# Optimization experiments

Hardware: AMD Instinct MI355X
Metric: run time of the kernel (lower is better)

Reference implementation:

```python
import jax, jax.numpy as jnp
import numpy as np

B, LR_DIM, G_DIM, K, D, T = 256, 1024, 512, 64, 256, 8
GRID = jnp.linspace(-4.0, 4.0, 41)  # registered buffer in torch module


def _mu_bell(x, c, a_bell, b_bell):
    # generalized bell membership, clamp(a,b) >= 1e-3 as in torch
    a = jnp.maximum(a_bell, 1e-3)
    b = jnp.maximum(b_bell, 1e-3)
    return 1.0 / (1.0 + jnp.abs((x - c) / a) ** (2.0 * b))


def _mu_s(x, a, b):
    eps = 1e-12
    a2 = jnp.minimum(a, b)
    b2 = jnp.maximum(a, b)
    mid = (a2 + b2) * 0.5
    up = 2.0 * ((x - a2) / (b2 - a2 + eps)) ** 2
    dn = 1.0 - 2.0 * ((b2 - x) / (b2 - a2 + eps)) ** 2
    y = jnp.where((x > a2) & (x <= mid), up, jnp.zeros_like(x))
    y = jnp.where((x > mid) & (x <= b2), dn, y)
    return jnp.where(x > b2, jnp.ones_like(x), y)


def _fuzzify(x, a_bell, b_bell):
    # x: (B,d) -> (B,2d)
    xs = 4.0 * jnp.tanh(x / 4.0)
    xb = _mu_bell(xs, 0.0, a_bell, b_bell)
    xS = _mu_s(xs, -1.0, 1.0)
    return jnp.concatenate([xb, xS], axis=-1)


def _defuzzify(rt, a_bell, b_bell):
    # rt: (B,2d) -> centroid (B,d)
    d = rt.shape[1] // 2
    rb, rs = rt[:, :d], rt[:, d:]
    g = GRID[None, None, :]                      # (1,1,G)
    c_b = 4.0 * jnp.tanh(rb)[..., None]          # (B,d,1)
    c_s = 4.0 * jnp.tanh(rs)[..., None]
    mu_b = _mu_bell(g, c_b, a_bell, b_bell)      # (B,d,G)
    a_s = jnp.clip(c_s - 1.0, -4.0, 4.0)
    b_s = jnp.clip(c_s + 1.0, -4.0, 4.0)
    mu_s = _mu_s(g, a_s, b_s)
    cen_b = (g * mu_b).sum(-1) / (mu_b.sum(-1) + 1e-12)
    cen_s = (g * mu_s).sum(-1) / (mu_s.sum(-1) + 1e-12)
    return 0.5 * cen_b + 0.5 * cen_s


def _forward(wsi_lr, genomics, FT, W_lr, b_lr, W_g, b_g, WqI, WqG, WkI, WkG,
             WvI, WvG, mlp_W1, mlp_b1, mlp_W2, mlp_b2, Wf, bf, Wi, bi, Vf, Vi,
             a_bell, b_bell):
    scale = jnp.float32(D) ** 0.5
    lr = wsi_lr @ W_lr + b_lr                    # (B,d)
    g = genomics @ W_g + b_g
    lr_f = _fuzzify(lr, a_bell, b_bell)          # (B,2d)
    g_f = _fuzzify(g, a_bell, b_bell)
    QI = lr_f @ WqI                              # (B,d), loop-invariant
    QG = g_f @ WqG
    Ft0 = jnp.broadcast_to(FT[None], (wsi_lr.shape[0],) + FT.shape)  # (B,K,d)

    def step(Ft, _):
        sI = jnp.einsum('bd,bkd->bk', QI, Ft @ WkI) / scale
        sG = jnp.einsum('bd,bkd->bk', QG, Ft @ WkG) / scale
        rtI = jnp.einsum('bk,bke->be', jax.nn.softmax(sI, axis=-1), Ft @ WvI)  # (B,2d)
        rtG = jnp.einsum('bk,bke->be', jax.nn.softmax(sG, axis=-1), Ft @ WvG)
        r = 0.5 * _defuzzify(rtI, a_bell, b_bell) + 0.5 * _defuzzify(rtG, a_bell, b_bell)
        rb = jnp.broadcast_to(r[:, None, :], Ft.shape)              # (B,K,d)
        x = Ft + rb
        F_tilde = jax.nn.gelu(x @ mlp_W1 + mlp_b1, approximate=False) @ mlp_W2 + mlp_b2 + x
        f_gate = jax.nn.sigmoid(rb @ Wf + bf + jnp.tanh(Ft @ Vf))
        i_gate = jax.nn.sigmoid(rb @ Wi + bi + jnp.tanh(Ft @ Vi))
        Ft_new = f_gate * Ft + i_gate * jnp.tanh(F_tilde)
        return Ft_new, Ft_new

    _, steps = jax.lax.scan(step, Ft0, None, length=T)
    # torch stores step `T-s` result at index s-1: list index 0 holds the LAST
    # computed state, index T-1 the first -> reverse chronological order
    return steps[::-1]  # (T,B,K,d)


def setup_inputs() -> dict:
    key = jax.random.key(0)
    ks = jax.random.split(key, 20)

    def rn(k, shape, scale):
        return jax.random.normal(k, shape, dtype=jnp.float32) * scale

    z = lambda *s: jnp.zeros(s, jnp.float32)
    return dict(
        wsi_lr=rn(ks[0], (B, LR_DIM), 1.0),
        genomics=rn(ks[1], (B, G_DIM), 1.0),
        FT=rn(ks[2], (K, D), 0.02),
        W_lr=rn(ks[3], (LR_DIM, D), LR_DIM ** -0.5), b_lr=z(D),
        W_g=rn(ks[4], (G_DIM, D), G_DIM ** -0.5), b_g=z(D),
        WqI=rn(ks[5], (2 * D, D), (2 * D) ** -0.5),
        WqG=rn(ks[6], (2 * D, D), (2 * D) ** -0.5),
        WkI=rn(ks[7], (D, D), D ** -0.5),
        WkG=rn(ks[8], (D, D), D ** -0.5),
        WvI=rn(ks[9], (D, 2 * D), D ** -0.5),
        WvG=rn(ks[10], (D, 2 * D), D ** -0.5),
        mlp_W1=rn(ks[11], (D, 2 * D), D ** -0.5), mlp_b1=z(2 * D),
        mlp_W2=rn(ks[12], (2 * D, D), (2 * D) ** -0.5), mlp_b2=z(D),
        Wf=rn(ks[13], (D, D), D ** -0.5), bf=z(D),
        Wi=rn(ks[14], (D, D), D ** -0.5), bi=z(D),
        Vf=rn(ks[15], (D, D), D ** -0.5),
        Vi=rn(ks[16], (D, D), D ** -0.5),
        a_bell=jnp.float32(1.0),
        b_bell=jnp.float32(2.0),
    )


def reference(wsi_lr, genomics, FT, W_lr, b_lr, W_g, b_g, WqI, WqG, WkI, WkG,
              WvI, WvG, mlp_W1, mlp_b1, mlp_W2, mlp_b2, Wf, bf, Wi, bi, Vf, Vi,
              a_bell, b_bell):
    return _forward(wsi_lr, genomics, FT, W_lr, b_lr, W_g, b_g, WqI, WqG, WkI,
                    WkG, WvI, WvG, mlp_W1, mlp_b1, mlp_W2, mlp_b2, Wf, bf, Wi,
                    bi, Vf, Vi, a_bell, b_bell)
```

## Files before the change

kernel.cpp:

```cpp
#include <hip/hip_runtime.h>
#include <hip/hip_bf16.h>

#define B_    256
#define K_    64
#define D_    256
#define T_    8
#define NROW  (B_*K_)

typedef short short8v __attribute__((ext_vector_type(8)));
typedef float f32x4  __attribute__((ext_vector_type(4)));

__device__ __forceinline__ float fexp2(float x) { return __builtin_amdgcn_exp2f(x); }
__device__ __forceinline__ float flog2(float x) { return __builtin_amdgcn_logf(x); }

__device__ __forceinline__ float sigmoid_f(float x) {
  return 1.f / (1.f + fexp2(x * -1.4426950408889634f));
}
__device__ __forceinline__ float tanh_fast(float x) {
  float xc = fminf(fmaxf(x, -30.f), 30.f);
  float t = fexp2(xc * 2.8853900817779268f);
  return (t - 1.f) / (t + 1.f);
}
__device__ __forceinline__ float gelu_f(float x) {
  return 0.5f * x * (1.f + erff(x * 0.70710678118654752440f));
}
__device__ __forceinline__ unsigned short f2bf(float x) {
  __hip_bfloat16 h = __float2bfloat16(x);
  return *reinterpret_cast<unsigned short*>(&h);
}
__device__ __forceinline__ float bfss(unsigned short s) {
  return __uint_as_float(((unsigned int)s) << 16);
}
__device__ __forceinline__ float muS_f(float x, float a2, float b2) {
  float mid = 0.5f * (a2 + b2);
  float inv = 1.f / (b2 - a2 + 1e-12f);
  if (x > b2)  return 1.f;
  if (x > mid) { float u = (b2 - x) * inv; return 1.f - 2.f * u * u; }
  if (x > a2)  { float u = (x - a2) * inv; return 2.f * u * u; }
  return 0.f;
}
__device__ __forceinline__ float pow_abs(float z, float e2b) {
  return fexp2(e2b * flog2(fabsf(z)));
}
__device__ __forceinline__ float defuzz_one(float rb_, float rs_, float ab, float bb) {
  float e2b = 2.f * bb;
  float inv_ab = 1.f / ab;
  float cb = 4.f * tanh_fast(rb_);
  float num = 0.f, den = 0.f;
  #pragma unroll
  for (int j = 0; j < 41; ++j) {
    float gj = -4.f + 0.2f * (float)j;
    float mu = 1.f / (1.f + pow_abs((gj - cb) * inv_ab, e2b));
    num += gj * mu; den += mu;
  }
  float cenb = num / (den + 1e-12f);
  float cs = 4.f * tanh_fast(rs_);
  float as_ = fminf(fmaxf(cs - 1.f, -4.f), 4.f);
  float bs_ = fminf(fmaxf(cs + 1.f, -4.f), 4.f);
  num = 0.f; den = 0.f;
  {
    float mid = 0.5f * (as_ + bs_);
    float inv = 1.f / (bs_ - as_ + 1e-12f);
    #pragma unroll
    for (int j = 0; j < 41; ++j) {
      float gj = -4.f + 0.2f * (float)j;
      float mu;
      if (gj > bs_)      mu = 1.f;
      else if (gj > mid) { float u = (bs_ - gj) * inv; mu = 1.f - 2.f * u * u; }
      else if (gj > as_) { float u = (gj - as_) * inv; mu = 2.f * u * u; }
      else               mu = 0.f;
      num += gj * mu; den += mu;
    }
  }
  float cens = num / (den + 1e-12f);
  return 0.5f * cenb + 0.5f * cens;
}

__global__ __launch_bounds__(256) void k_convert(
    const float* __restrict__ W1, const float* __restrict__ Vf, const float* __restrict__ Vi,
    const float* __restrict__ W2, const float* __restrict__ FT,
    const float* __restrict__ WkI, const float* __restrict__ WkG,
    const float* __restrict__ WvI, const float* __restrict__ WvG,
    const float* __restrict__ Wf,  const float* __restrict__ Wi,
    unsigned short* __restrict__ B1t, unsigned short* __restrict__ W2t,
    unsigned short* __restrict__ FTbf,
    float* __restrict__ WkIt, float* __restrict__ WkGt,
    unsigned short* __restrict__ Wv2, unsigned short* __restrict__ WB)
{
  int idx = blockIdx.x * 256 + threadIdx.x;
  if (idx < 262144) {
    int n = idx >> 8, k = idx & 255;
    float v = (n < 512) ? W1[(size_t)k*512 + n]
            : (n < 768) ? Vf[(size_t)k*256 + (n-512)]
                        : Vi[(size_t)k*256 + (n-768)];
    B1t[idx] = f2bf(v);
  } else if (idx < 393216) {
    int j = idx - 262144;
    int n = j >> 9, k = j & 511;
    W2t[j] = f2bf(W2[(size_t)k*256 + n]);
  } else if (idx < 409600) {
    int j = idx - 393216;
    FTbf[j] = f2bf(FT[j]);
  } else if (idx < 475136) {
    int j = idx - 409600;
    int k = j >> 8, n = j & 255;
    WkIt[j] = WkI[(size_t)n*256 + k];
  } else if (idx < 540672) {
    int j = idx - 475136;
    int k = j >> 8, n = j & 255;
    WkGt[j] = WkG[(size_t)n*256 + k];
  } else if (idx < 802816) {
    int j = idx - 540672;
    int d = j >> 10, c = j & 1023;
    float v = (c < 512) ? WvI[(size_t)d*512 + c] : WvG[(size_t)d*512 + (c-512)];
    Wv2[j] = f2bf(v);
  } else if (idx < 1064960) {
    int j = idx - 802816;
    int d = j >> 10, c = j & 1023;
    float v = (c < 512) ? W1[(size_t)d*512 + c]
            : (c < 768) ? Wf[(size_t)d*256 + (c-512)]
                        : Wi[(size_t)d*256 + (c-768)];
    WB[j] = f2bf(v);
  }
}

__global__ __launch_bounds__(256) void k_pre_lin(
    const float* __restrict__ wsi, const float* __restrict__ gen,
    const float* __restrict__ W_lr, const float* __restrict__ b_lr,
    const float* __restrict__ W_g,  const float* __restrict__ b_g,
    const float* __restrict__ a_p,  const float* __restrict__ b_p,
    float* __restrict__ lrf, float* __restrict__ gf)
{
  int g_ix = blockIdx.x;
  int half = g_ix >> 4, tile = g_ix & 15;
  int bx = tile & 3, by = tile >> 2;
  int n0 = bx * 64, m0 = by * 64;
  const float* A    = half ? gen  : wsi;
  const float* Bm   = half ? W_g  : W_lr;
  const float* bias = half ? b_g  : b_lr;
  float* outp       = half ? gf   : lrf;
  int KK            = half ? 512  : 1024;
  float ab = fmaxf(a_p[0], 0.001f), bb = fmaxf(b_p[0], 0.001f);
  float e2b = 2.f * bb, inv_ab = 1.f / ab;

  __shared__ float As[16][64];
  __shared__ float Bs[16][64];
  int tid = threadIdx.x, tx = tid & 15, ty = tid >> 4;
  float acc[4][4] = {};
  int am = tid >> 2, ak = (tid & 3) * 4;
  int bk = tid >> 4, bn = (tid & 15) * 4;
  const float* arow = A + (size_t)(m0 + am) * KK;
  for (int k0 = 0; k0 < KK; k0 += 16) {
    float4 av = *(const float4*)(arow + k0 + ak);
    As[ak+0][am] = av.x; As[ak+1][am] = av.y; As[ak+2][am] = av.z; As[ak+3][am] = av.w;
    *(float4*)&Bs[bk][bn] = *(const float4*)(Bm + (size_t)(k0 + bk) * 256 + n0 + bn);
    __syncthreads();
    #pragma unroll
    for (int kk = 0; kk < 16; ++kk) {
      float a0 = As[kk][ty*4+0], a1 = As[kk][ty*4+1], a2 = As[kk][ty*4+2], a3 = As[kk][ty*4+3];
      float b0 = Bs[kk][tx*4+0], b1 = Bs[kk][tx*4+1], b2 = Bs[kk][tx*4+2], b3 = Bs[kk][tx*4+3];
      acc[0][0]=fmaf(a0,b0,acc[0][0]); acc[0][1]=fmaf(a0,b1,acc[0][1]); acc[0][2]=fmaf(a0,b2,acc[0][2]); acc[0][3]=fmaf(a0,b3,acc[0][3]);
      acc[1][0]=fmaf(a1,b0,acc[1][0]); acc[1][1]=fmaf(a1,b1,acc[1][1]); acc[1][2]=fmaf(a1,b2,acc[1][2]); acc[1][3]=fmaf(a1,b3,acc[1][3]);
      acc[2][0]=fmaf(a2,b0,acc[2][0]); acc[2][1]=fmaf(a2,b1,acc[2][1]); acc[2][2]=fmaf(a2,b2,acc[2][2]); acc[2][3]=fmaf(a2,b3,acc[2][3]);
      acc[3][0]=fmaf(a3,b0,acc[3][0]); acc[3][1]=fmaf(a3,b1,acc[3][1]); acc[3][2]=fmaf(a3,b2,acc[3][2]); acc[3][3]=fmaf(a3,b3,acc[3][3]);
    }
    __syncthreads();
  }
  #pragma unroll
  for (int i = 0; i < 4; ++i) {
    int row = m0 + ty*4 + i;
    #pragma unroll
    for (int j = 0; j < 4; ++j) {
      int col = n0 + tx*4 + j;
      float v = acc[i][j] + bias[col];
      float xs = 4.f * tanh_fast(v * 0.25f);
      outp[(size_t)row*512 + col]       = 1.f / (1.f + pow_abs(xs * inv_ab, e2b));
      outp[(size_t)row*512 + col + 256] = muS_f(xs, -1.f, 1.f);
    }
  }
}

__global__ __launch_bounds__(256) void k_pre_q(
    const float* __restrict__ lrf, const float* __restrict__ gf,
    const float* __restrict__ WqI, const float* __restrict__ WqG,
    float* __restrict__ QI, float* __restrict__ QG)
{
  int g_ix = blockIdx.x;
  int half = g_ix >> 4, tile = g_ix & 15;
  int bx = tile & 3, by = tile >> 2;
  int n0 = bx * 64, m0 = by * 64;
  const float* A  = half ? gf  : lrf;
  const float* Bm = half ? WqG : WqI;
  float* outp     = half ? QG  : QI;

  __shared__ float As[16][64];
  __shared__ float Bs[16][64];
  int tid = threadIdx.x, tx = tid & 15, ty = tid >> 4;
  float acc[4][4] = {};
  int am = tid >> 2, ak = (tid & 3) * 4;
  int bk = tid >> 4, bn = (tid & 15) * 4;
  const float* arow = A + (size_t)(m0 + am) * 512;
  for (int k0 = 0; k0 < 512; k0 += 16) {
    float4 av = *(const float4*)(arow + k0 + ak);
    As[ak+0][am] = av.x; As[ak+1][am] = av.y; As[ak+2][am] = av.z; As[ak+3][am] = av.w;
    *(float4*)&Bs[bk][bn] = *(const float4*)(Bm + (size_t)(k0 + bk) * 256 + n0 + bn);
    __syncthreads();
    #pragma unroll
    for (int kk = 0; kk < 16; ++kk) {
      float a0 = As[kk][ty*4+0], a1 = As[kk][ty*4+1], a2 = As[kk][ty*4+2], a3 = As[kk][ty*4+3];
      float b0 = Bs[kk][tx*4+0], b1 = Bs[kk][tx*4+1], b2 = Bs[kk][tx*4+2], b3 = Bs[kk][tx*4+3];
      acc[0][0]=fmaf(a0,b0,acc[0][0]); acc[0][1]=fmaf(a0,b1,acc[0][1]); acc[0][2]=fmaf(a0,b2,acc[0][2]); acc[0][3]=fmaf(a0,b3,acc[0][3]);
      acc[1][0]=fmaf(a1,b0,acc[1][0]); acc[1][1]=fmaf(a1,b1,acc[1][1]); acc[1][2]=fmaf(a1,b2,acc[1][2]); acc[1][3]=fmaf(a1,b3,acc[1][3]);
      acc[2][0]=fmaf(a2,b0,acc[2][0]); acc[2][1]=fmaf(a2,b1,acc[2][1]); acc[2][2]=fmaf(a2,b2,acc[2][2]); acc[2][3]=fmaf(a2,b3,acc[2][3]);
      acc[3][0]=fmaf(a3,b0,acc[3][0]); acc[3][1]=fmaf(a3,b1,acc[3][1]); acc[3][2]=fmaf(a3,b2,acc[3][2]); acc[3][3]=fmaf(a3,b3,acc[3][3]);
    }
    __syncthreads();
  }
  #pragma unroll
  for (int i = 0; i < 4; ++i) {
    float4 v = make_float4(acc[i][0], acc[i][1], acc[i][2], acc[i][3]);
    *(float4*)(outp + (size_t)(m0 + ty*4 + i) * 256 + n0 + tx*4) = v;
  }
}

__global__ __launch_bounds__(256) void k_pre_qp(
    const float* __restrict__ QI, const float* __restrict__ QG,
    const float* __restrict__ WkIt, const float* __restrict__ WkGt,
    float* __restrict__ qIp, float* __restrict__ qGp)
{
  int g_ix = blockIdx.x;
  int half = g_ix >> 4, tile = g_ix & 15;
  int bx = tile & 3, by = tile >> 2;
  int n0 = bx * 64, m0 = by * 64;
  const float* A  = half ? QG   : QI;
  const float* Bm = half ? WkGt : WkIt;
  float* outp     = half ? qGp  : qIp;

  __shared__ float As[16][64];
  __shared__ float Bs[16][64];
  int tid = threadIdx.x, tx = tid & 15, ty = tid >> 4;
  float acc[4][4] = {};
  int am = tid >> 2, ak = (tid & 3) * 4;
  int bk = tid >> 4, bn = (tid & 15) * 4;
  const float* arow = A + (size_t)(m0 + am) * 256;
  for (int k0 = 0; k0 < 256; k0 += 16) {
    float4 av = *(const float4*)(arow + k0 + ak);
    As[ak+0][am] = av.x; As[ak+1][am] = av.y; As[ak+2][am] = av.z; As[ak+3][am] = av.w;
    *(float4*)&Bs[bk][bn] = *(const float4*)(Bm + (size_t)(k0 + bk) * 256 + n0 + bn);
    __syncthreads();
    #pragma unroll
    for (int kk = 0; kk < 16; ++kk) {
      float a0 = As[kk][ty*4+0], a1 = As[kk][ty*4+1], a2 = As[kk][ty*4+2], a3 = As[kk][ty*4+3];
      float b0 = Bs[kk][tx*4+0], b1 = Bs[kk][tx*4+1], b2 = Bs[kk][tx*4+2], b3 = Bs[kk][tx*4+3];
      acc[0][0]=fmaf(a0,b0,acc[0][0]); acc[0][1]=fmaf(a0,b1,acc[0][1]); acc[0][2]=fmaf(a0,b2,acc[0][2]); acc[0][3]=fmaf(a0,b3,acc[0][3]);
      acc[1][0]=fmaf(a1,b0,acc[1][0]); acc[1][1]=fmaf(a1,b1,acc[1][1]); acc[1][2]=fmaf(a1,b2,acc[1][2]); acc[1][3]=fmaf(a1,b3,acc[1][3]);
      acc[2][0]=fmaf(a2,b0,acc[2][0]); acc[2][1]=fmaf(a2,b1,acc[2][1]); acc[2][2]=fmaf(a2,b2,acc[2][2]); acc[2][3]=fmaf(a2,b3,acc[2][3]);
      acc[3][0]=fmaf(a3,b0,acc[3][0]); acc[3][1]=fmaf(a3,b1,acc[3][1]); acc[3][2]=fmaf(a3,b2,acc[3][2]); acc[3][3]=fmaf(a3,b3,acc[3][3]);
    }
    __syncthreads();
  }
  #pragma unroll
  for (int i = 0; i < 4; ++i) {
    float4 v = make_float4(acc[i][0], acc[i][1], acc[i][2], acc[i][3]);
    *(float4*)(outp + (size_t)(m0 + ty*4 + i) * 256 + n0 + tx*4) = v;
  }
}

__global__ __launch_bounds__(512) void k_scan(
    const unsigned short* __restrict__ FTbf, const float* __restrict__ FTf,
    const float* __restrict__ qIp, const float* __restrict__ qGp,
    const unsigned short* __restrict__ Wv2, const unsigned short* __restrict__ WB,
    const float* __restrict__ b1, const float* __restrict__ bfv,
    const float* __restrict__ biv, const float* __restrict__ b2,
    const unsigned short* __restrict__ B1t, const unsigned short* __restrict__ W2t,
    const float* __restrict__ a_p, const float* __restrict__ b_p,
    unsigned short* __restrict__ Gf, unsigned short* __restrict__ Gi,
    float* __restrict__ out)
{
  __shared__ __align__(16) short Fs[64*264];
  __shared__ __align__(16) short Bstage[64*264];
  __shared__ __align__(16) short Wstage[256*72];
  __shared__ __align__(16) short A2ch[64*72];
  __shared__ float qv[512];
  __shared__ float red[512];
  __shared__ float prl[128];
  __shared__ float ftb[512];
  __shared__ float rL[256];
  __shared__ float rWall[1024];

  int b = blockIdx.x, tid = threadIdx.x;
  int w = tid >> 6, lane = tid & 63, lr = lane & 15, lh = lane >> 4;
  int rg = w & 3, cg = w >> 2;
  float ab = fmaxf(a_p[0], 0.001f), bb = fmaxf(b_p[0], 0.001f);

  #pragma unroll
  for (int p = 0; p < 4; ++p) {
    int idx = (p*512 + tid) * 8;
    int row = idx >> 8, col = idx & 255;
    *(float4*)&Fs[row*264 + col] = *(const float4*)&FTbf[idx];
  }
  qv[tid] = (tid < 256) ? qIp[(size_t)b*256 + tid] : qGp[(size_t)b*256 + tid - 256];
  __syncthreads();

  const float* Fprev = nullptr;
  for (int st = 0; st < T_; ++st) {
    float* Fout = out + (size_t)(7 - st) * NROW * 256;

    {
      int which = tid >> 8, tt = tid & 255, k = tt & 63, part = tt >> 6;
      const unsigned int* frow = (const unsigned int*)&Fs[k*264 + part*64];
      const float* q0 = qv + which*256 + part*64;
      float s0 = 0.f;
      #pragma unroll
      for (int d2 = 0; d2 < 32; ++d2) {
        unsigned int pr = frow[d2];
        float f0 = __uint_as_float(pr << 16);
        float f1 = __uint_as_float(pr & 0xffff0000u);
        s0 = fmaf(f1, q0[2*d2+1], fmaf(f0, q0[2*d2], s0));
      }
      red[which*256 + tt] = s0;
    }
    __syncthreads();
    if (tid < 128) {
      int which = tid >> 6, kk = tid & 63;
      const float* rp = red + which*256;
      float s = (rp[kk] + rp[64+kk] + rp[128+kk] + rp[192+kk]) * (1.f/16.f);
      float m = s;
      for (int off = 32; off; off >>= 1) m = fmaxf(m, __shfl_xor(m, off, 64));
      float e = fexp2((s - m) * 1.4426950408889634f);
      float sum = e;
      for (int off = 32; off; off >>= 1) sum += __shfl_xor(sum, off, 64);
      prl[which*64 + kk] = e / sum;
    }
    __syncthreads();
    {
      int which = tid >> 8, tt = tid & 255;
      const float* pp = prl + which*64;
      float f0 = 0.f;
      #pragma unroll 8
      for (int kk = 0; kk < 64; ++kk)
        f0 = fmaf(pp[kk], bfss((unsigned short)Fs[kk*264 + tt]), f0);
      ftb[which*256 + tt] = f0;
    }
    __syncthreads();
    {
      int half = tid >> 8, tt = tid & 255;
      const float* fb = ftb + half*256;
      const unsigned short* wv = Wv2 + half*512 + tt;
      float a0 = 0.f, a1 = 0.f;
      #pragma unroll 4
      for (int d = 0; d < 256; ++d) {
        float fv = fb[d];
        a0 = fmaf(fv, bfss(wv[(size_t)d*1024]),       a0);
        a1 = fmaf(fv, bfss(wv[(size_t)d*1024 + 256]), a1);
      }
      red[half*256 + tt] = defuzz_one(a0, a1, ab, bb);
    }
    __syncthreads();
    if (tid < 256) rL[tid] = 0.5f * (red[tid] + red[256 + tid]);
    __syncthreads();
    {
      float w0 = 0.f, w1 = 0.f;
      const unsigned short* wb0 = WB + tid;
      #pragma unroll 4
      for (int d = 0; d < 256; ++d) {
        float rv = rL[d];
        w0 = fmaf(rv, bfss(wb0[(size_t)d*1024]),       w0);
        w1 = fmaf(rv, bfss(wb0[(size_t)d*1024 + 512]), w1);
      }
      rWall[tid]       = w0 + b1[tid];
      rWall[512 + tid] = w1 + ((tid < 256) ? bfv[tid] : biv[tid - 256]);
    }
    __syncthreads();

    for (int c = 8; c < 16; ++c) {
      #pragma unroll
      for (int p = 0; p < 4; ++p) {
        int idx = (p*512 + tid) * 8;
        int row = idx >> 8, col = idx & 255;
        *(float4*)&Bstage[row*264 + col] = *(const float4*)&B1t[(size_t)c*16384 + idx];
      }
      __syncthreads();
      #pragma unroll
      for (int f = 0; f < 2; ++f) {
        f32x4 acc = {0.f,0.f,0.f,0.f};
        int nb = cg*32 + f*16;
        #pragma unroll
        for (int ks = 0; ks < 8; ++ks) {
          short8v av = *(const short8v*)&Fs[(rg*16 + lr)*264 + ks*32 + lh*8];
          short8v bv = *(const short8v*)&Bstage[(nb + lr)*264 + ks*32 + lh*8];
          acc = __builtin_amdgcn_mfma_f32_16x16x32_bf16(av, bv, acc, 0, 0, 0);
        }
        int gc = c*64 + nb + lr;
        float add = rWall[gc];
        int cc = gc - 512;
        #pragma unroll
        for (int r = 0; r < 4; ++r) {
          int row = b*64 + rg*16 + lh*4 + r;
          unsigned short val = f2bf(sigmoid_f(add + tanh_fast(acc[r])));
          if (cc < 256) Gf[(size_t)row*256 + cc]       = val;
          else          Gi[(size_t)row*256 + cc - 256] = val;
        }
      }
      __syncthreads();
    }

    f32x4 O[8];
    #pragma unroll
    for (int nn = 0; nn < 8; ++nn) { O[nn][0]=0.f; O[nn][1]=0.f; O[nn][2]=0.f; O[nn][3]=0.f; }
    for (int c = 0; c < 8; ++c) {
      #pragma unroll
      for (int p = 0; p < 4; ++p) {
        int idx = (p*512 + tid) * 8;
        int row = idx >> 8, col = idx & 255;
        *(float4*)&Bstage[row*264 + col] = *(const float4*)&B1t[(size_t)c*16384 + idx];
      }
      #pragma unroll
      for (int p = 0; p < 4; ++p) {
        int idx = (p*512 + tid) * 8;
        int n = idx >> 6, kk = idx & 63;
        *(float4*)&Wstage[n*72 + kk] = *(const float4*)&W2t[(size_t)n*512 + c*64 + kk];
      }
      __syncthreads();
      #pragma unroll
      for (int f = 0; f < 2; ++f) {
        f32x4 acc = {0.f,0.f,0.f,0.f};
        int nb = cg*32 + f*16;
        #pragma unroll
        for (int ks = 0; ks < 8; ++ks) {
          short8v av = *(const short8v*)&Fs[(rg*16 + lr)*264 + ks*32 + lh*8];
          short8v bv = *(const short8v*)&Bstage[(nb + lr)*264 + ks*32 + lh*8];
          acc = __builtin_amdgcn_mfma_f32_16x16x32_bf16(av, bv, acc, 0, 0, 0);
        }
        int gc = c*64 + nb + lr;
        float add = rWall[gc];
        #pragma unroll
        for (int r = 0; r < 4; ++r)
          A2ch[(rg*16 + lh*4 + r)*72 + nb + lr] = f2bf(gelu_f(acc[r] + add));
      }
      __syncthreads();
      #pragma unroll
      for (int ks2 = 0; ks2 < 2; ++ks2) {
        short8v av = *(const short8v*)&A2ch[(rg*16 + lr)*72 + ks2*32 + lh*8];
        #pragma unroll
        for (int nn = 0; nn < 8; ++nn) {
          short8v bv = *(const short8v*)&Wstage[(cg*128 + nn*16 + lr)*72 + ks2*32 + lh*8];
          O[nn] = __builtin_amdgcn_mfma_f32_16x16x32_bf16(av, bv, O[nn], 0, 0, 0);
        }
      }
      __syncthreads();
    }

    #pragma unroll
    for (int nn = 0; nn < 8; ++nn) {
      int col = cg*128 + nn*16 + lr;
      float b2c = b2[col], rv = rL[col];
      #pragma unroll
      for (int r = 0; r < 4; ++r) {
        int rowl = rg*16 + lh*4 + r;
        int row = b*64 + rowl;
        float Ftv = (st == 0) ? FTf[rowl*256 + col] : Fprev[(size_t)row*256 + col];
        float ftld = O[nn][r] + b2c + Ftv + rv;
        float fg = bfss(Gf[(size_t)row*256 + col]);
        float ig = bfss(Gi[(size_t)row*256 + col]);
        float ov = fg * Ftv + ig * tanh_fast(ftld);
        Fout[(size_t)row*256 + col] = ov;
        Fs[rowl*264 + col] = f2bf(ov);
      }
    }
    Fprev = Fout;
    __syncthreads();
  }
}

extern "C" void kernel_launch(void* const* d_in, const int* in_sizes, int n_in,
                              void* d_out, int out_size, void* d_ws, size_t ws_size,
                              hipStream_t stream)
{
  (void)in_sizes; (void)n_in; (void)out_size; (void)ws_size;
  const float* wsi  = (const float*)d_in[0];
  const float* gen  = (const float*)d_in[1];
  const float* FT   = (const float*)d_in[2];
  const float* W_lr = (const float*)d_in[3];
  const float* b_lr = (const float*)d_in[4];
  const float* W_g  = (const float*)d_in[5];
  const float* b_g  = (const float*)d_in[6];
  const float* WqI  = (const float*)d_in[7];
  const float* WqG  = (const float*)d_in[8];
  const float* WkI  = (const float*)d_in[9];
  const float* WkG  = (const float*)d_in[10];
  const float* WvI  = (const float*)d_in[11];
  const float* WvG  = (const float*)d_in[12];
  const float* W1   = (const float*)d_in[13];
  const float* b1   = (const float*)d_in[14];
  const float* W2   = (const float*)d_in[15];
  const float* b2   = (const float*)d_in[16];
  const float* Wf   = (const float*)d_in[17];
  const float* bf   = (const float*)d_in[18];
  const float* Wi   = (const float*)d_in[19];
  const float* bi   = (const float*)d_in[20];
  const float* Vf   = (const float*)d_in[21];
  const float* Vi   = (const float*)d_in[22];
  const float* a_p  = (const float*)d_in[23];
  const float* b_p  = (const float*)d_in[24];

  float* out = (float*)d_out;
  float* ws  = (float*)d_ws;
  float* qIp   = ws;
  float* qGp   = qIp   + 65536;
  float* lrf   = qGp   + 65536;
  float* gf    = lrf   + 131072;
  float* QI    = gf    + 131072;
  float* QG    = QI    + 65536;
  float* WkIt  = QG    + 65536;
  float* WkGt  = WkIt  + 65536;
  unsigned short* Gfb  = (unsigned short*)(WkGt + 65536);
  unsigned short* Gib  = Gfb  + 4194304;
  unsigned short* FTbf = Gib  + 4194304;
  unsigned short* B1t  = FTbf + 16384;
  unsigned short* W2t  = B1t  + 262144;
  unsigned short* Wv2  = W2t  + 131072;
  unsigned short* WB   = Wv2  + 262144;

  k_convert<<<4160, 256, 0, stream>>>(W1, Vf, Vi, W2, FT, WkI, WkG, WvI, WvG, Wf, Wi,
                                      B1t, W2t, FTbf, WkIt, WkGt, Wv2, WB);
  k_pre_lin<<<32, 256, 0, stream>>>(wsi, gen, W_lr, b_lr, W_g, b_g, a_p, b_p, lrf, gf);
  k_pre_q<<<32, 256, 0, stream>>>(lrf, gf, WqI, WqG, QI, QG);
  k_pre_qp<<<32, 256, 0, stream>>>(QI, QG, WkIt, WkGt, qIp, qGp);

  k_scan<<<256, 512, 0, stream>>>(FTbf, FT, qIp, qGp, Wv2, WB,
                                  b1, bf, bi, b2, B1t, W2t, a_p, b_p,
                                  Gfb, Gib, out);
}
```

Measured before the change: 870.3 us.

## Prefetch next weight chunk into registers during MFMA loops; stagger score reads

The gate and MLP chunk loops now load the next chunk of B1t (and W2t) from global memory into registers right after the barrier, so the global loads overlap with the current chunk's MFMA work instead of stalling before each LDS store. The attention score loop also rotates its start index by k to spread LDS bank accesses. The change adds register pressure (8 extra float4 per thread in the MLP loop), which could lower occupancy or cause spills.

```diff
diff --git a/kernel.cpp b/kernel.cpp
--- a/kernel.cpp
+++ b/kernel.cpp
@@ -312,7 +312,8 @@
       const float* q0 = qv + which*256 + part*64;
       float s0 = 0.f;
       #pragma unroll
-      for (int d2 = 0; d2 < 32; ++d2) {
+      for (int d2i = 0; d2i < 32; ++d2i) {
+        int d2 = (d2i + k) & 31;
         unsigned int pr = frow[d2];
         float f0 = __uint_as_float(pr << 16);
         float f1 = __uint_as_float(pr & 0xffff0000u);
@@ -369,86 +370,113 @@
         w1 = fmaf(rv, bfss(wb0[(size_t)d*1024 + 512]), w1);
       }
       rWall[tid]       = w0 + b1[tid];
-      rWall[512 + tid] = w1 + ((tid < 256) ? bfv[tid] : biv[tid - 256]);
-    }
-    __syncthreads();
-
-    for (int c = 8; c < 16; ++c) {
+      int tt = tid & 255;
+      rWall[512 + tid] = w1 + ((tid < 256) ? bfv[tt] : biv[tt]);
+    }
+    __syncthreads();
+
+    {
+      float4 pfB[4];
+      #pragma unroll
+      for (int p = 0; p < 4; ++p)
+        pfB[p] = *(const float4*)&B1t[(size_t)8*16384 + (p*512 + tid)*8];
+      for (int c = 8; c < 16; ++c) {
+        #pragma unroll
+        for (int p = 0; p < 4; ++p) {
+          int idx = (p*512 + tid) * 8;
+          int row = idx >> 8, col = idx & 255;
+          *(float4*)&Bstage[row*264 + col] = pfB[p];
+        }
+        __syncthreads();
+        if (c < 15) {
+          #pragma unroll
+          for (int p = 0; p < 4; ++p)
+            pfB[p] = *(const float4*)&B1t[(size_t)(c+1)*16384 + (p*512 + tid)*8];
+        }
+        #pragma unroll
+        for (int f = 0; f < 2; ++f) {
+          f32x4 acc = {0.f,0.f,0.f,0.f};
+          int nb = cg*32 + f*16;
+          #pragma unroll
+          for (int ks = 0; ks < 8; ++ks) {
+            short8v av = *(const short8v*)&Fs[(rg*16 + lr)*264 + ks*32 + lh*8];
+            short8v bv = *(const short8v*)&Bstage[(nb + lr)*264 + ks*32 + lh*8];
+            acc = __builtin_amdgcn_mfma_f32_16x16x32_bf16(av, bv, acc, 0, 0, 0);
+          }
+          int gc = c*64 + nb + lr;
+          float add = rWall[gc];
+          int cc = gc - 512;
+          #pragma unroll
+          for (int r = 0; r < 4; ++r) {
+            int row = b*64 + rg*16 + lh*4 + r;
+            unsigned short val = f2bf(sigmoid_f(add + tanh_fast(acc[r])));
+            if (cc < 256) Gf[(size_t)row*256 + cc]       = val;
+            else          Gi[(size_t)row*256 + cc - 256] = val;
+          }
+        }
+        __syncthreads();
+      }
+    }
+
+    f32x4 O[8];
+    #pragma unroll
+    for (int nn = 0; nn < 8; ++nn) { O[nn][0]=0.f; O[nn][1]=0.f; O[nn][2]=0.f; O[nn][3]=0.f; }
+    {
+      float4 pfB[4], pfW[4];
       #pragma unroll
       for (int p = 0; p < 4; ++p) {
         int idx = (p*512 + tid) * 8;
-        int row = idx >> 8, col = idx & 255;
-        *(float4*)&Bstage[row*264 + col] = *(const float4*)&B1t[(size_t)c*16384 + idx];
-      }
-      __syncthreads();
-      #pragma unroll
-      for (int f = 0; f < 2; ++f) {
-        f32x4 acc = {0.f,0.f,0.f,0.f};
-        int nb = cg*32 + f*16;
+        pfB[p] = *(const float4*)&B1t[idx];
+        int n = idx >> 6, kk = idx & 63;
+        pfW[p] = *(const float4*)&W2t[(size_t)n*512 + kk];
+      }
+      for (int c = 0; c < 8; ++c) {
         #pragma unroll
-        for (int ks = 0; ks < 8; ++ks) {
-          short8v av = *(const short8v*)&Fs[(rg*16 + lr)*264 + ks*32 + lh*8];
-          short8v bv = *(const short8v*)&Bstage[(nb + lr)*264 + ks*32 + lh*8];
-          acc = __builtin_amdgcn_mfma_f32_16x16x32_bf16(av, bv, acc, 0, 0, 0);
-        }
-        int gc = c*64 + nb + lr;
-        float add = rWall[gc];
-        int cc = gc - 512;
+        for (int p = 0; p < 4; ++p) {
+          int idx = (p*512 + tid) * 8;
+          int row = idx >> 8, col = idx & 255;
+          *(float4*)&Bstage[row*264 + col] = pfB[p];
+          int n = idx >> 6, kk = idx & 63;
+          *(float4*)&Wstage[n*72 + kk] = pfW[p];
+        }
+        __syncthreads();
+        if (c < 7) {
+          #pragma unroll
+          for (int p = 0; p < 4; ++p) {
+            int idx = (p*512 + tid) * 8;
+            pfB[p] = *(const float4*)&B1t[(size_t)(c+1)*16384 + idx];
+            int n = idx >> 6, kk = idx & 63;
+            pfW[p] = *(const float4*)&W2t[(size_t)n*512 + (c+1)*64 + kk];
+          }
+        }
         #pragma unroll
-        for (int r = 0; r < 4; ++r) {
-          int row = b*64 + rg*16 + lh*4 + r;
-          unsigned short val = f2bf(sigmoid_f(add + tanh_fast(acc[r])));
-          if (cc < 256) Gf[(size_t)row*256 + cc]       = val;
-          else          Gi[(size_t)row*256 + cc - 256] = val;
-        }
-      }
-      __syncthreads();
-    }
-
-    f32x4 O[8];
-    #pragma unroll
-    for (int nn = 0; nn < 8; ++nn) { O[nn][0]=0.f; O[nn][1]=0.f; O[nn][2]=0.f; O[nn][3]=0.f; }
-    for (int c = 0; c < 8; ++c) {
-      #pragma unroll
-      for (int p = 0; p < 4; ++p) {
-        int idx = (p*512 + tid) * 8;
-        int row = idx >> 8, col = idx & 255;
-        *(float4*)&Bstage[row*264 + col] = *(const float4*)&B1t[(size_t)c*16384 + idx];
-      }
-      #pragma unroll
-      for (int p = 0; p < 4; ++p) {
-        int idx = (p*512 + tid) * 8;
-        int n = idx >> 6, kk = idx & 63;
-        *(float4*)&Wstage[n*72 + kk] = *(const float4*)&W2t[(size_t)n*512 + c*64 + kk];
-      }
-      __syncthreads();
-      #pragma unroll
-      for (int f = 0; f < 2; ++f) {
-        f32x4 acc = {0.f,0.f,0.f,0.f};
-        int nb = cg*32 + f*16;
+        for (int f = 0; f < 2; ++f) {
+          f32x4 acc = {0.f,0.f,0.f,0.f};
+          int nb = cg*32 + f*16;
+          #pragma unroll
+          for (int ks = 0; ks < 8; ++ks) {
+            short8v av = *(const short8v*)&Fs[(rg*16 + lr)*264 + ks*32 + lh*8];
+            short8v bv = *(const short8v*)&Bstage[(nb + lr)*264 + ks*32 + lh*8];
+            acc = __builtin_amdgcn_mfma_f32_16x16x32_bf16(av, bv, acc, 0, 0, 0);
+          }
+          int gc = c*64 + nb + lr;
+          float add = rWall[gc];
+          #pragma unroll
+          for (int r = 0; r < 4; ++r)
+            A2ch[(rg*16 + lh*4 + r)*72 + nb + lr] = f2bf(gelu_f(acc[r] + add));
+        }
+        __syncthreads();
         #pragma unroll
-        for (int ks = 0; ks < 8; ++ks) {
-          short8v av = *(const short8v*)&Fs[(rg*16 + lr)*264 + ks*32 + lh*8];
-          short8v bv = *(const short8v*)&Bstage[(nb + lr)*264 + ks*32 + lh*8];
-          acc = __builtin_amdgcn_mfma_f32_16x16x32_bf16(av, bv, acc, 0, 0, 0);
-        }
-        int gc = c*64 + nb + lr;
-        float add = rWall[gc];
-        #pragma unroll
-        for (int r = 0; r < 4; ++r)
-          A2ch[(rg*16 + lh*4 + r)*72 + nb + lr] = f2bf(gelu_f(acc[r] + add));
-      }
-      __syncthreads();
-      #pragma unroll
-      for (int ks2 = 0; ks2 < 2; ++ks2) {
-        short8v av = *(const short8v*)&A2ch[(rg*16 + lr)*72 + ks2*32 + lh*8];
-        #pragma unroll
-        for (int nn = 0; nn < 8; ++nn) {
-          short8v bv = *(const short8v*)&Wstage[(cg*128 + nn*16 + lr)*72 + ks2*32 + lh*8];
-          O[nn] = __builtin_amdgcn_mfma_f32_16x16x32_bf16(av, bv, O[nn], 0, 0, 0);
-        }
-      }
-      __syncthreads();
+        for (int ks2 = 0; ks2 < 2; ++ks2) {
+          short8v av = *(const short8v*)&A2ch[(rg*16 + lr)*72 + ks2*32 + lh*8];
+          #pragma unroll
+          for (int nn = 0; nn < 8; ++nn) {
+            short8v bv = *(const short8v*)&Wstage[(cg*128 + nn*16 + lr)*72 + ks2*32 + lh*8];
+            O[nn] = __builtin_amdgcn_mfma_f32_16x16x32_bf16(av, bv, O[nn], 0, 0, 0);
+          }
+        }
+        __syncthreads();
+      }
     }
 
     #pragma unroll
```

Result: slower. 2.025 ms (+132.7%).
